# Optimization experiments

Hardware: AMD Instinct MI355X
Metric: run time of the kernel (lower is better)

The kernel has to match this reference:

```python
import jax, jax.numpy as jnp
import numpy as np

B, L, DIM, H, HD = 1, 2048, 2048, 16, 128  # head_dim = DIM // H; RoPE pairs = HD // 2


def setup_inputs() -> dict:
    key = jax.random.key(0)
    ks = jax.random.split(key, 6)
    x = jax.random.normal(ks[0], (B, L, DIM), dtype=jnp.float32)
    pe = jax.random.normal(ks[1], (1, 1, L, HD // 2, 2, 2), dtype=jnp.float32)
    qkv_w = jax.random.normal(ks[2], (3 * DIM, DIM), dtype=jnp.float32) * 0.02
    q_scale = jnp.ones((HD,), dtype=jnp.float32)
    k_scale = jnp.ones((HD,), dtype=jnp.float32)
    proj_w = jax.random.normal(ks[3], (DIM, DIM), dtype=jnp.float32) * 0.02
    proj_b = jnp.zeros((DIM,), dtype=jnp.float32)
    return {"x": x, "pe": pe, "qkv_w": qkv_w, "q_scale": q_scale,
            "k_scale": k_scale, "proj_w": proj_w, "proj_b": proj_b}


def _rmsnorm(t, scale):
    # per-head-dim RMSNorm, eps=1e-6, computed in fp32 (inputs already fp32)
    rrms = jax.lax.rsqrt(jnp.mean(t * t, axis=-1, keepdims=True) + 1e-6)
    return t * rrms * scale


def _apply_rope(q, k, pe):
    def rot(t):
        t_ = t.reshape(*t.shape[:-1], -1, 1, 2)  # [B,H,L,HD/2,1,2]
        out = pe[..., 0] * t_[..., 0] + pe[..., 1] * t_[..., 1]  # [B,H,L,HD/2,2]
        return out.reshape(t.shape)
    return rot(q), rot(k)


def reference(x, pe, qkv_w, q_scale, k_scale, proj_w, proj_b):
    b, l, _ = x.shape
    qkv = jnp.einsum('bld,ed->ble', x, qkv_w)  # [B, L, 3*DIM]
    qkv = qkv.reshape(b, l, 3, H, HD)
    # 'B L (K H D) -> K B H L D'
    qkv = jnp.transpose(qkv, (2, 0, 3, 1, 4))
    q, k, v = qkv[0], qkv[1], qkv[2]  # each [B, H, L, HD]
    q = _rmsnorm(q, q_scale)
    k = _rmsnorm(k, k_scale)
    q, k = _apply_rope(q, k, pe)
    scale = 1.0 / jnp.sqrt(jnp.asarray(HD, dtype=q.dtype))
    scores = jnp.einsum('bhqd,bhkd->bhqk', q, k) * scale
    attn = jax.nn.softmax(scores, axis=-1)
    out = jnp.einsum('bhqk,bhkd->bhqd', attn, v)  # [B, H, L, HD]
    out = jnp.transpose(out, (0, 2, 1, 3)).reshape(b, l, H * HD)  # 'B H L D -> B L (H D)'
    return jnp.einsum('bld,ed->ble', out, proj_w) + proj_b
```

## Files before the change

kernel.cpp:

```cpp
#include <hip/hip_runtime.h>
#include <hip/hip_bf16.h>
#include <math.h>

#define L_SEQ 2048
#define DIM   2048
#define NH    16
#define HD    128
#define TDIM  6144

typedef __attribute__((ext_vector_type(8))) short short8;
typedef __attribute__((ext_vector_type(4))) float f32x4;
typedef __attribute__((ext_vector_type(4))) unsigned int u32x4;

__device__ __forceinline__ void gl_lds16(const void* g, void* l) {
  __builtin_amdgcn_global_load_lds(
      (const __attribute__((address_space(1))) unsigned int*)g,
      (__attribute__((address_space(3))) unsigned int*)l, 16, 0, 0);
}

__device__ __forceinline__ short bf16bits(float x) {
  __hip_bfloat16 h = __float2bfloat16(x);
  return *(short*)&h;
}

__device__ __forceinline__ float bits2f(short s) {
  unsigned int u = ((unsigned int)(unsigned short)s) << 16;
  return __uint_as_float(u);
}

__device__ __forceinline__ unsigned int pack_bf16(float a, float b) {
  __hip_bfloat162 h = __float22bfloat162_rn(make_float2(a, b));
  return *(unsigned int*)&h;
}

__global__ __launch_bounds__(256)
void cast2_bf16(const float* __restrict__ a, __hip_bfloat16* __restrict__ oa,
                const float* __restrict__ b, __hip_bfloat16* __restrict__ ob) {
  int i = (blockIdx.x * 256 + threadIdx.x) * 8;
  const float* src;
  __hip_bfloat16* dst;
  int off;
  if (i < DIM * DIM) { src = a; dst = oa; off = i; }
  else               { src = b; dst = ob; off = i - DIM * DIM; }
  float4 v0 = *(const float4*)(src + off);
  float4 v1 = *(const float4*)(src + off + 4);
  short8 o;
  o[0] = bf16bits(v0.x); o[1] = bf16bits(v0.y); o[2] = bf16bits(v0.z); o[3] = bf16bits(v0.w);
  o[4] = bf16bits(v1.x); o[5] = bf16bits(v1.y); o[6] = bf16bits(v1.z); o[7] = bf16bits(v1.w);
  *(short8*)(dst + off) = o;
}

__global__ __launch_bounds__(256)
void cast_bf16(const float* __restrict__ in, __hip_bfloat16* __restrict__ out, int n) {
  int i = (blockIdx.x * 256 + threadIdx.x) * 8;
  if (i >= n) return;
  float4 a = *(const float4*)(in + i);
  float4 b = *(const float4*)(in + i + 4);
  short8 o;
  o[0] = bf16bits(a.x); o[1] = bf16bits(a.y); o[2] = bf16bits(a.z); o[3] = bf16bits(a.w);
  o[4] = bf16bits(b.x); o[5] = bf16bits(b.y); o[6] = bf16bits(b.z); o[7] = bf16bits(b.w);
  *(short8*)(out + i) = o;
}

#define QKV_N 6144
#define QKV_K 2048

__global__ __launch_bounds__(512, 2)
void gemm_qkv_256(const __hip_bfloat16* __restrict__ A,
                  const __hip_bfloat16* __restrict__ B,
                  __hip_bfloat16* __restrict__ C) {
  extern __shared__ char smem[];
  const int tid  = threadIdx.x;
  const int lane = tid & 63, w = tid >> 6;
  const int l15  = lane & 15, quad = lane >> 4;
  const int wm   = w >> 2, wn = w & 3;

  const int orig = blockIdx.x;
  const int by = orig & 7;
  const int bx = orig >> 3;
  const int m0 = by * 256, n0 = bx * 256;

  const int ar0 = tid >> 2,         aq0 = tid & 3;
  const int ar1 = (512 + tid) >> 2, aq1 = (512 + tid) & 3;
  const __hip_bfloat16* pA0 = A + (size_t)(m0 + ar0) * QKV_K + aq0 * 8;
  const __hip_bfloat16* pA1 = A + (size_t)(m0 + ar1) * QKV_K + aq1 * 8;
  const __hip_bfloat16* pB0 = B + (size_t)(n0 + ar0) * QKV_K + aq0 * 8;
  const __hip_bfloat16* pB1 = B + (size_t)(n0 + ar1) * QKV_K + aq1 * 8;
  const int dst0 = w * 1024;

  f32x4 acc[8][4];
#pragma unroll
  for (int mi = 0; mi < 8; ++mi)
#pragma unroll
    for (int ni = 0; ni < 4; ++ni) acc[mi][ni] = (f32x4){0.f, 0.f, 0.f, 0.f};

  const int aoff = ((wm * 128 + l15) * 32 + quad * 8) * 2;
  const int boff = ((wn * 64 + l15) * 32 + quad * 8) * 2;

#pragma unroll
  for (int p = 0; p < 3; ++p) {
    char* Sp = smem + p * 32768;
    gl_lds16(pA0 + p * 32, Sp + dst0);
    gl_lds16(pA1 + p * 32, Sp + dst0 + 8192);
    gl_lds16(pB0 + p * 32, Sp + 16384 + dst0);
    gl_lds16(pB1 + p * 32, Sp + 16384 + dst0 + 8192);
  }
  asm volatile("s_waitcnt vmcnt(8)\n\ts_barrier" ::: "memory");

  for (int tb = 0; tb < 64; tb += 4) {
#pragma unroll
    for (int u = 0; u < 4; ++u) {
      const int t  = tb + u;
      const char* As = smem + u * 32768;
      const char* Bs = As + 16384;
      const int tn = (t + 3) & 63;
      char* Sn = smem + ((u + 3) & 3) * 32768;

      short8 a[8];
#pragma unroll
      for (int mi = 0; mi < 8; ++mi)
        a[mi] = *(const short8*)(As + aoff + mi * 1024);
      short8 b0 = *(const short8*)(Bs + boff);
      short8 b1 = *(const short8*)(Bs + boff + 1024);
      gl_lds16(pA0 + tn * 32, Sn + dst0);
      gl_lds16(pA1 + tn * 32, Sn + dst0 + 8192);
      __builtin_amdgcn_s_barrier();
      __builtin_amdgcn_s_setprio(1);
#pragma unroll
      for (int mi = 0; mi < 8; ++mi) {
        acc[mi][0] = __builtin_amdgcn_mfma_f32_16x16x32_bf16(a[mi], b0, acc[mi][0], 0, 0, 0);
        acc[mi][1] = __builtin_amdgcn_mfma_f32_16x16x32_bf16(a[mi], b1, acc[mi][1], 0, 0, 0);
      }
      __builtin_amdgcn_s_setprio(0);
      __builtin_amdgcn_s_barrier();

      short8 b2 = *(const short8*)(Bs + boff + 2048);
      short8 b3 = *(const short8*)(Bs + boff + 3072);
      gl_lds16(pB0 + tn * 32, Sn + 16384 + dst0);
      gl_lds16(pB1 + tn * 32, Sn + 16384 + dst0 + 8192);
      asm volatile("s_waitcnt vmcnt(8)\n\ts_barrier" ::: "memory");
      __builtin_amdgcn_s_setprio(1);
#pragma unroll
      for (int mi = 0; mi < 8; ++mi) {
        acc[mi][2] = __builtin_amdgcn_mfma_f32_16x16x32_bf16(a[mi], b2, acc[mi][2], 0, 0, 0);
        acc[mi][3] = __builtin_amdgcn_mfma_f32_16x16x32_bf16(a[mi], b3, acc[mi][3], 0, 0, 0);
      }
      __builtin_amdgcn_s_setprio(0);
      __builtin_amdgcn_s_barrier();
    }
  }

  const int crow = m0 + wm * 128 + quad * 4;
  const int ccol = n0 + wn * 64 + l15;
#pragma unroll
  for (int mi = 0; mi < 8; ++mi)
#pragma unroll
    for (int ni = 0; ni < 4; ++ni)
#pragma unroll
      for (int r = 0; r < 4; ++r)
        C[(size_t)(crow + mi * 16 + r) * QKV_N + ccol + ni * 16] =
            __float2bfloat16(acc[mi][ni][r]);
}

__global__ __launch_bounds__(256)
void qkv_epilogue(const __hip_bfloat16* __restrict__ C,
                  const float* __restrict__ q_scale, const float* __restrict__ k_scale,
                  const float* __restrict__ pe,
                  __hip_bfloat16* __restrict__ Qb, __hip_bfloat16* __restrict__ Kb,
                  __hip_bfloat16* __restrict__ Vt) {
  const int bid = blockIdx.x;
  const int t = threadIdx.x;
  if (bid < 512) {
    const int sec = bid >> 8;
    const int h   = (bid >> 4) & 15;
    const int rb  = bid & 15;
    const float* scale = sec ? k_scale : q_scale;
    const float qmul = sec ? 1.0f : 0.08838834764831845f;
    __hip_bfloat16* dst = sec ? Kb : Qb;

    const int row = t >> 1, half = t & 1;
    const int l = rb * 128 + row;
    const __hip_bfloat16* grow = C + (size_t)l * TDIM + sec * DIM + h * HD + half * 64;

    float ss = 0.f;
#pragma unroll
    for (int c8 = 0; c8 < 64; c8 += 8) {
      short8 v8 = *(const short8*)(grow + c8);
#pragma unroll
      for (int j = 0; j < 8; ++j) { float f = bits2f(v8[j]); ss += f * f; }
    }
    ss += __shfl_xor(ss, 1);
    const float rrms = rsqrtf(ss * (1.f / 128.f) + 1e-6f);

    const float* perow = pe + (size_t)l * 256 + half * 128;
    __hip_bfloat16* drow = dst + ((size_t)h * L_SEQ + l) * HD + half * 64;

#pragma unroll
    for (int c8 = 0; c8 < 64; c8 += 8) {
      short8 v8 = *(const short8*)(grow + c8);
      float f[8];
#pragma unroll
      for (int j = 0; j < 8; ++j)
        f[j] = bits2f(v8[j]) * rrms * scale[half * 64 + c8 + j];
      short8 o;
#pragma unroll
      for (int p = 0; p < 4; ++p) {
        float4 pp = *(const float4*)(perow + c8 * 2 + p * 4);
        float e = f[2 * p], od = f[2 * p + 1];
        o[2 * p]     = bf16bits((pp.x * e + pp.y * od) * qmul);
        o[2 * p + 1] = bf16bits((pp.z * e + pp.w * od) * qmul);
      }
      *(short8*)(drow + c8) = o;
    }
  } else {
    __shared__ short Tt[128 * 72];
    const int vb = bid - 512;
    const int h = vb >> 5, lb = vb & 31;
    const int l0 = lb * 64;
#pragma unroll
    for (int k = 0; k < 4; ++k) {
      int idx = t + k * 256;
      int row = idx >> 4, c = idx & 15;
      short8 v = *(const short8*)(C + (size_t)(l0 + row) * TDIM + 2 * DIM + h * HD + c * 8);
#pragma unroll
      for (int j = 0; j < 8; ++j) Tt[(c * 8 + j) * 72 + row] = v[j];
    }
    __syncthreads();
    const int d = t >> 1, lh = t & 1;
    __hip_bfloat16* vrow = Vt + ((size_t)h * HD + d) * L_SEQ + l0 + lh * 32;
#pragma unroll
    for (int k = 0; k < 4; ++k) {
      short8 o = *(const short8*)&Tt[d * 72 + lh * 32 + k * 8];
      *(short8*)(vrow + k * 8) = o;
    }
  }
}

__global__ __launch_bounds__(256)
void gemm_proj(const __hip_bfloat16* __restrict__ A, const __hip_bfloat16* __restrict__ B,
               const float* __restrict__ bias, float* __restrict__ C,
               int M, int N, int K) {
  const int n0 = blockIdx.x * 128, m0 = blockIdx.y * 128;
  const int t = threadIdx.x, lane = t & 63, w = t >> 6;
  const int l15 = lane & 15, quad = lane >> 4;
  const int wm = (w & 1) * 64, wn = (w >> 1) * 64;

  __shared__ __align__(16) __hip_bfloat16 As[128 * 32];
  __shared__ __align__(16) __hip_bfloat16 Bs[128 * 32];

  f32x4 acc[4][4];
#pragma unroll
  for (int mt = 0; mt < 4; ++mt)
#pragma unroll
    for (int nt = 0; nt < 4; ++nt) acc[mt][nt] = (f32x4){0.f, 0.f, 0.f, 0.f};

  const int arow  = lane >> 2;
  const int acol8 = (lane & 3) * 8;
  const __hip_bfloat16* Ab = A + (size_t)(m0 + w * 16 + arow) * K + acol8;
  const __hip_bfloat16* Bb = B + (size_t)(n0 + w * 16 + arow) * K + acol8;
  __hip_bfloat16* As_base = As + (size_t)(w * 16) * 32;
  __hip_bfloat16* Bs_base = Bs + (size_t)(w * 16) * 32;

  for (int kb = 0; kb < K; kb += 32) {
    gl_lds16(Ab + kb,                As_base);
    gl_lds16(Ab + kb + (size_t)64*K, As_base + 64 * 32);
    gl_lds16(Bb + kb,                Bs_base);
    gl_lds16(Bb + kb + (size_t)64*K, Bs_base + 64 * 32);
    __syncthreads();

    short8 am[4], bn[4];
#pragma unroll
    for (int mt = 0; mt < 4; ++mt)
      am[mt] = *(const short8*)&As[(size_t)(wm + mt*16 + l15) * 32 + quad * 8];
#pragma unroll
    for (int nt = 0; nt < 4; ++nt)
      bn[nt] = *(const short8*)&Bs[(size_t)(wn + nt*16 + l15) * 32 + quad * 8];
#pragma unroll
    for (int mt = 0; mt < 4; ++mt)
#pragma unroll
      for (int nt = 0; nt < 4; ++nt)
        acc[mt][nt] = __builtin_amdgcn_mfma_f32_16x16x32_bf16(am[mt], bn[nt], acc[mt][nt], 0, 0, 0);
    __syncthreads();
  }

#pragma unroll
  for (int mt = 0; mt < 4; ++mt)
#pragma unroll
    for (int nt = 0; nt < 4; ++nt) {
      int col = n0 + wn + nt * 16 + l15;
#pragma unroll
      for (int r = 0; r < 4; ++r) {
        int row = m0 + wm + mt * 16 + quad * 4 + r;
        C[(size_t)row * N + col] = acc[mt][nt][r] + bias[col];
      }
    }
}

#define NZ 4
#define ZLEN (L_SEQ / NZ)

__global__ __launch_bounds__(256, 4)
void attn_mfma(const __hip_bfloat16* __restrict__ Qb,
               const __hip_bfloat16* __restrict__ Kb,
               const __hip_bfloat16* __restrict__ Vt,
               __hip_bfloat16* __restrict__ Opart, float2* __restrict__ ml) {
  const int orig = blockIdx.x;
  const int wg   = (orig & 7) * 256 + (orig >> 3);
  const int h    = wg >> 7;
  const int rem  = wg & 127;
  const int z    = rem >> 5;
  const int q0   = (rem & 31) * 64;
  const int t  = threadIdx.x;
  const int lane = t & 63, w = t >> 6;
  const int l15 = lane & 15, quad = lane >> 4;
  const int sw = l15 & 7;

  __shared__ __align__(16) __hip_bfloat16 Ks[64 * 128];
  __shared__ __align__(16) __hip_bfloat16 Vs[128 * 64];

  const __hip_bfloat16* kbase = Kb + (size_t)h * L_SEQ * HD;
  const __hip_bfloat16* vbase = Vt + (size_t)h * HD * L_SEQ;

  short8 aq[4];
  {
    const __hip_bfloat16* qbase = Qb + ((size_t)h * L_SEQ + q0 + w * 16 + l15) * HD;
#pragma unroll
    for (int ks = 0; ks < 4; ++ks)
      aq[ks] = *(const short8*)(qbase + ks * 32 + quad * 8);
  }

  f32x4 o[8];
#pragma unroll
  for (int n2 = 0; n2 < 8; ++n2) o[n2] = (f32x4){0.f, 0.f, 0.f, 0.f};
  float m_run = -1e30f, l_run = 0.f;

  for (int kt = 0; kt < ZLEN / 64; ++kt) {
    const int k0 = z * ZLEN + kt * 64;
#pragma unroll
    for (int i = 0; i < 4; ++i) {
      int krow = w * 16 + i * 4 + (lane >> 4);
      int kch  = (lane & 15) ^ (krow & 7);
      gl_lds16(kbase + (size_t)(k0 + krow) * HD + kch * 8,
               &Ks[(w * 16 + i * 4) * 128]);
    }
#pragma unroll
    for (int i = 0; i < 4; ++i) {
      int vrow = w * 32 + i * 8 + (lane >> 3);
      int vch  = (lane & 7) ^ (vrow & 7);
      gl_lds16(vbase + (size_t)vrow * L_SEQ + k0 + vch * 8,
               &Vs[(w * 32 + i * 8) * 64]);
    }
    __syncthreads();

    f32x4 s[4];
#pragma unroll
    for (int nt = 0; nt < 4; ++nt) s[nt] = (f32x4){0.f, 0.f, 0.f, 0.f};
    __builtin_amdgcn_s_setprio(1);
#pragma unroll
    for (int ks = 0; ks < 4; ++ks) {
      short8 bk[4];
#pragma unroll
      for (int nt = 0; nt < 4; ++nt)
        bk[nt] = *(const short8*)&Ks[(nt * 16 + l15) * 128 + ((ks * 4 + quad) ^ sw) * 8];
#pragma unroll
      for (int nt = 0; nt < 4; ++nt)
        s[nt] = __builtin_amdgcn_mfma_f32_16x16x32_bf16(bk[nt], aq[ks], s[nt], 0, 0, 0);
    }
    __builtin_amdgcn_s_setprio(0);

    float mx0 = fmaxf(fmaxf(s[0][0], s[0][1]), fmaxf(s[0][2], s[0][3]));
    float mx1 = fmaxf(fmaxf(s[1][0], s[1][1]), fmaxf(s[1][2], s[1][3]));
    float mx2 = fmaxf(fmaxf(s[2][0], s[2][1]), fmaxf(s[2][2], s[2][3]));
    float mx3 = fmaxf(fmaxf(s[3][0], s[3][1]), fmaxf(s[3][2], s[3][3]));
    float rm = fmaxf(fmaxf(mx0, mx1), fmaxf(mx2, mx3));
    rm = fmaxf(rm, __shfl_xor(rm, 16));
    rm = fmaxf(rm, __shfl_xor(rm, 32));

    if (!__all(rm <= m_run + 8.f)) {
      float mnew = fmaxf(m_run, rm);
      float alpha = __expf(m_run - mnew);
      m_run = mnew;
      l_run *= alpha;
      float alpha_r[4];
#pragma unroll
      for (int r = 0; r < 4; ++r) alpha_r[r] = __shfl(alpha, quad * 4 + r);
#pragma unroll
      for (int n2 = 0; n2 < 8; ++n2)
#pragma unroll
        for (int r = 0; r < 4; ++r) o[n2][r] *= alpha_r[r];
    }

    float sum = 0.f;
#pragma unroll
    for (int nt = 0; nt < 4; ++nt)
#pragma unroll
      for (int r = 0; r < 4; ++r) {
        float p = __expf(s[nt][r] - m_run);
        s[nt][r] = p;
        sum += p;
      }
    sum += __shfl_xor(sum, 16);
    sum += __shfl_xor(sum, 32);
    l_run += sum;

    unsigned int pk[4][2];
#pragma unroll
    for (int nt = 0; nt < 4; ++nt) {
      pk[nt][0] = pack_bf16(s[nt][0], s[nt][1]);
      pk[nt][1] = pack_bf16(s[nt][2], s[nt][3]);
    }
    short8 ap[2];
#pragma unroll
    for (int ks2 = 0; ks2 < 2; ++ks2) {
      u32x4 a32;
#pragma unroll
      for (int jp = 0; jp < 4; ++jp) {
        int quad_src = (quad & 1) * 2 + (jp >> 1);
        int src = (quad_src << 4) | l15;
        int rp = jp & 1;
        unsigned int v0 = __shfl((int)pk[2 * ks2 + 0][rp], src);
        unsigned int v1 = __shfl((int)pk[2 * ks2 + 1][rp], src);
        a32[jp] = (quad >> 1) ? v1 : v0;
      }
      ap[ks2] = *(short8*)&a32;
    }

    __builtin_amdgcn_s_setprio(1);
#pragma unroll
    for (int ks2 = 0; ks2 < 2; ++ks2)
#pragma unroll
      for (int n2 = 0; n2 < 8; ++n2) {
        short8 bv = *(const short8*)&Vs[(n2 * 16 + l15) * 64 + ((ks2 * 4 + quad) ^ sw) * 8];
        o[n2] = __builtin_amdgcn_mfma_f32_16x16x32_bf16(ap[ks2], bv, o[n2], 0, 0, 0);
      }
    __builtin_amdgcn_s_setprio(0);

    __syncthreads();
  }

  const size_t rb = (size_t)(z * NH + h) * L_SEQ + q0 + w * 16;
  float linv[4];
#pragma unroll
  for (int r = 0; r < 4; ++r) linv[r] = 1.f / __shfl(l_run, quad * 4 + r);
#pragma unroll
  for (int r = 0; r < 4; ++r) {
    size_t row = rb + quad * 4 + r;
#pragma unroll
    for (int n2 = 0; n2 < 8; ++n2)
      Opart[row * HD + n2 * 16 + l15] = __float2bfloat16(o[n2][r] * linv[r]);
  }
  if (quad == 0) ml[rb + l15] = make_float2(m_run, l_run);
}

__global__ __launch_bounds__(256)
void attn_combine4(const __hip_bfloat16* __restrict__ Opart,
                   const float2* __restrict__ ml,
                   __hip_bfloat16* __restrict__ out) {
  const int h  = blockIdx.y;
  const int q  = blockIdx.x * 16 + (threadIdx.x >> 4);
  const int d8 = (threadIdx.x & 15) * 8;
  size_t idx[NZ];
  float2 a[NZ];
#pragma unroll
  for (int zz = 0; zz < NZ; ++zz) {
    idx[zz] = ((size_t)zz * NH + h) * L_SEQ + q;
    a[zz] = ml[idx[zz]];
  }
  float M = fmaxf(fmaxf(a[0].x, a[1].x), fmaxf(a[2].x, a[3].x));
  float wz[NZ];
  float tot = 0.f;
#pragma unroll
  for (int zz = 0; zz < NZ; ++zz) {
    wz[zz] = __expf(a[zz].x - M) * a[zz].y;
    tot += wz[zz];
  }
  float inv = 1.f / tot;
  float acc[8] = {0.f, 0.f, 0.f, 0.f, 0.f, 0.f, 0.f, 0.f};
#pragma unroll
  for (int zz = 0; zz < NZ; ++zz) {
    short8 ov = *(const short8*)&Opart[idx[zz] * HD + d8];
#pragma unroll
    for (int j = 0; j < 8; ++j) acc[j] += wz[zz] * bits2f(ov[j]);
  }
  short8 r;
#pragma unroll
  for (int j = 0; j < 8; ++j) r[j] = bf16bits(acc[j] * inv);
  *(short8*)&out[(size_t)q * DIM + h * HD + d8] = r;
}

extern "C" void kernel_launch(void* const* d_in, const int* in_sizes, int n_in,
                              void* d_out, int out_size, void* d_ws, size_t ws_size,
                              hipStream_t stream) {
  const float* x       = (const float*)d_in[0];
  const float* pe      = (const float*)d_in[1];
  const float* qkv_w   = (const float*)d_in[2];
  const float* q_scale = (const float*)d_in[3];
  const float* k_scale = (const float*)d_in[4];
  const float* proj_w  = (const float*)d_in[5];
  const float* proj_b  = (const float*)d_in[6];
  float* out = (float*)d_out;

  char* base = (char*)d_ws;
  __hip_bfloat16* xb       = (__hip_bfloat16*)base;
  __hip_bfloat16* wb       = (__hip_bfloat16*)(base + 8388608);
  __hip_bfloat16* Cq       = (__hip_bfloat16*)(base + 33554432);
  __hip_bfloat16* Qb       = (__hip_bfloat16*)base;
  __hip_bfloat16* Kb       = (__hip_bfloat16*)(base + 8388608);
  __hip_bfloat16* Vt       = (__hip_bfloat16*)(base + 16777216);
  __hip_bfloat16* Opart    = (__hip_bfloat16*)(base + 33554432);
  float2*         ml       = (float2*)(base + 25165824);
  __hip_bfloat16* attn_out = (__hip_bfloat16*)base;
  __hip_bfloat16* pwb      = (__hip_bfloat16*)(base + 33554432);

  static bool attr_done = false;
  if (!attr_done) {
    hipFuncSetAttribute((const void*)gemm_qkv_256,
                        hipFuncAttributeMaxDynamicSharedMemorySize, 131072);
    attr_done = true;
  }

  cast2_bf16<<<dim3((DIM * DIM + TDIM * DIM) / (256 * 8)), 256, 0, stream>>>(
      x, xb, qkv_w, wb);

  gemm_qkv_256<<<dim3((TDIM / 256) * (L_SEQ / 256)), 512, 131072, stream>>>(xb, wb, Cq);

  qkv_epilogue<<<dim3(1024), 256, 0, stream>>>(Cq, q_scale, k_scale, pe, Qb, Kb, Vt);

  attn_mfma<<<dim3(NZ * NH * (L_SEQ / 64)), 256, 0, stream>>>(Qb, Kb, Vt, Opart, ml);

  attn_combine4<<<dim3(L_SEQ / 16, NH), 256, 0, stream>>>(Opart, ml, attn_out);

  cast_bf16<<<dim3(DIM * DIM / (256 * 8)), 256, 0, stream>>>(proj_w, pwb, DIM * DIM);

  gemm_proj<<<dim3(DIM / 128, DIM / 128), 256, 0, stream>>>(
      attn_out, pwb, proj_b, out, L_SEQ, DIM, DIM);
}
```

Measured before the change: 329.1 us.

## Switch attention to 32x32x16 MFMA with 128-row query tiles and permlane swap

The attention kernel now uses 32x32x16 bf16 MFMAs instead of 16x16x32, and each wave owns 32 query rows, so a block covers 128 queries and the grid is halved. The P-to-A-operand conversion uses v_permlane32_swap instead of several shuffles, and one lane owns one query row, which removes most cross-lane reductions. The output is staged through LDS so each row goes to global memory as coalesced 16-byte stores. Each block now reuses every K/V tile for twice as many queries, but register pressure rises and occupancy is lowered to 3 blocks per CU.

Result: faster. 318.6 us (-3.2%).

```diff
diff --git a/kernel.cpp b/kernel.cpp
--- a/kernel.cpp
+++ b/kernel.cpp
@@ -10,6 +10,7 @@
 
 typedef __attribute__((ext_vector_type(8))) short short8;
 typedef __attribute__((ext_vector_type(4))) float f32x4;
+typedef __attribute__((ext_vector_type(16))) float f32x16;
 typedef __attribute__((ext_vector_type(4))) unsigned int u32x4;
 
 __device__ __forceinline__ void gl_lds16(const void* g, void* l) {
@@ -299,21 +300,21 @@
 #define NZ 4
 #define ZLEN (L_SEQ / NZ)
 
-__global__ __launch_bounds__(256, 4)
+__global__ __launch_bounds__(256, 3)
 void attn_mfma(const __hip_bfloat16* __restrict__ Qb,
                const __hip_bfloat16* __restrict__ Kb,
                const __hip_bfloat16* __restrict__ Vt,
                __hip_bfloat16* __restrict__ Opart, float2* __restrict__ ml) {
   const int orig = blockIdx.x;
-  const int wg   = (orig & 7) * 256 + (orig >> 3);
-  const int h    = wg >> 7;
-  const int rem  = wg & 127;
-  const int z    = rem >> 5;
-  const int q0   = (rem & 31) * 64;
-  const int t  = threadIdx.x;
+  const int wg   = (orig & 7) * 128 + (orig >> 3);
+  const int h    = wg >> 6;
+  const int rem  = wg & 63;
+  const int z    = rem >> 4;
+  const int q0   = (rem & 15) * 128;
+  const int t    = threadIdx.x;
   const int lane = t & 63, w = t >> 6;
-  const int l15 = lane & 15, quad = lane >> 4;
-  const int sw = l15 & 7;
+  const int l31  = lane & 31;
+  const int u    = lane >> 5;
 
   __shared__ __align__(16) __hip_bfloat16 Ks[64 * 128];
   __shared__ __align__(16) __hip_bfloat16 Vs[128 * 64];
@@ -321,17 +322,19 @@
   const __hip_bfloat16* kbase = Kb + (size_t)h * L_SEQ * HD;
   const __hip_bfloat16* vbase = Vt + (size_t)h * HD * L_SEQ;
 
-  short8 aq[4];
+  short8 aq[8];
   {
-    const __hip_bfloat16* qbase = Qb + ((size_t)h * L_SEQ + q0 + w * 16 + l15) * HD;
-#pragma unroll
-    for (int ks = 0; ks < 4; ++ks)
-      aq[ks] = *(const short8*)(qbase + ks * 32 + quad * 8);
-  }
-
-  f32x4 o[8];
-#pragma unroll
-  for (int n2 = 0; n2 < 8; ++n2) o[n2] = (f32x4){0.f, 0.f, 0.f, 0.f};
+    const __hip_bfloat16* qb = Qb + ((size_t)h * L_SEQ + q0 + w * 32 + l31) * HD + u * 8;
+#pragma unroll
+    for (int hh = 0; hh < 8; ++hh)
+      aq[hh] = *(const short8*)(qb + hh * 16);
+  }
+
+  f32x16 o[4];
+#pragma unroll
+  for (int dt = 0; dt < 4; ++dt)
+#pragma unroll
+    for (int r = 0; r < 16; ++r) o[dt][r] = 0.f;
   float m_run = -1e30f, l_run = 0.f;
 
   for (int kt = 0; kt < ZLEN / 64; ++kt) {
@@ -352,104 +355,105 @@
     }
     __syncthreads();
 
-    f32x4 s[4];
-#pragma unroll
-    for (int nt = 0; nt < 4; ++nt) s[nt] = (f32x4){0.f, 0.f, 0.f, 0.f};
-    __builtin_amdgcn_s_setprio(1);
-#pragma unroll
-    for (int ks = 0; ks < 4; ++ks) {
-      short8 bk[4];
-#pragma unroll
-      for (int nt = 0; nt < 4; ++nt)
-        bk[nt] = *(const short8*)&Ks[(nt * 16 + l15) * 128 + ((ks * 4 + quad) ^ sw) * 8];
-#pragma unroll
-      for (int nt = 0; nt < 4; ++nt)
-        s[nt] = __builtin_amdgcn_mfma_f32_16x16x32_bf16(bk[nt], aq[ks], s[nt], 0, 0, 0);
-    }
-    __builtin_amdgcn_s_setprio(0);
-
-    float mx0 = fmaxf(fmaxf(s[0][0], s[0][1]), fmaxf(s[0][2], s[0][3]));
-    float mx1 = fmaxf(fmaxf(s[1][0], s[1][1]), fmaxf(s[1][2], s[1][3]));
-    float mx2 = fmaxf(fmaxf(s[2][0], s[2][1]), fmaxf(s[2][2], s[2][3]));
-    float mx3 = fmaxf(fmaxf(s[3][0], s[3][1]), fmaxf(s[3][2], s[3][3]));
-    float rm = fmaxf(fmaxf(mx0, mx1), fmaxf(mx2, mx3));
-    rm = fmaxf(rm, __shfl_xor(rm, 16));
-    rm = fmaxf(rm, __shfl_xor(rm, 32));
-
-    if (!__all(rm <= m_run + 8.f)) {
-      float mnew = fmaxf(m_run, rm);
-      float alpha = __expf(m_run - mnew);
-      m_run = mnew;
-      l_run *= alpha;
-      float alpha_r[4];
-#pragma unroll
-      for (int r = 0; r < 4; ++r) alpha_r[r] = __shfl(alpha, quad * 4 + r);
-#pragma unroll
-      for (int n2 = 0; n2 < 8; ++n2)
-#pragma unroll
-        for (int r = 0; r < 4; ++r) o[n2][r] *= alpha_r[r];
-    }
-
-    float sum = 0.f;
-#pragma unroll
-    for (int nt = 0; nt < 4; ++nt)
-#pragma unroll
-      for (int r = 0; r < 4; ++r) {
-        float p = __expf(s[nt][r] - m_run);
-        s[nt][r] = p;
+#pragma unroll
+    for (int ks = 0; ks < 2; ++ks) {
+      const int krow = ks * 32 + l31;
+      const char* krowp = (const char*)Ks + krow * 256;
+      const int ksw = krow & 7;
+      f32x16 s;
+#pragma unroll
+      for (int r = 0; r < 16; ++r) s[r] = 0.f;
+      __builtin_amdgcn_s_setprio(1);
+#pragma unroll
+      for (int hh = 0; hh < 8; ++hh) {
+        short8 ak = *(const short8*)(krowp + ((hh * 2 + u) ^ ksw) * 16);
+        s = __builtin_amdgcn_mfma_f32_32x32x16_bf16(ak, aq[hh], s, 0, 0, 0);
+      }
+      __builtin_amdgcn_s_setprio(0);
+
+      float rm = s[0];
+#pragma unroll
+      for (int r = 1; r < 16; ++r) rm = fmaxf(rm, s[r]);
+      rm = fmaxf(rm, __shfl_xor(rm, 32));
+
+      if (!__all(rm <= m_run + 8.f)) {
+        float mnew = fmaxf(m_run, rm);
+        float alpha = __expf(m_run - mnew);
+        m_run = mnew;
+        l_run *= alpha;
+#pragma unroll
+        for (int dt = 0; dt < 4; ++dt)
+#pragma unroll
+          for (int r = 0; r < 16; ++r) o[dt][r] *= alpha;
+      }
+
+      float sum = 0.f;
+#pragma unroll
+      for (int r = 0; r < 16; ++r) {
+        float p = __expf(s[r] - m_run);
+        s[r] = p;
         sum += p;
       }
-    sum += __shfl_xor(sum, 16);
-    sum += __shfl_xor(sum, 32);
-    l_run += sum;
-
-    unsigned int pk[4][2];
-#pragma unroll
-    for (int nt = 0; nt < 4; ++nt) {
-      pk[nt][0] = pack_bf16(s[nt][0], s[nt][1]);
-      pk[nt][1] = pack_bf16(s[nt][2], s[nt][3]);
-    }
-    short8 ap[2];
-#pragma unroll
-    for (int ks2 = 0; ks2 < 2; ++ks2) {
-      u32x4 a32;
-#pragma unroll
-      for (int jp = 0; jp < 4; ++jp) {
-        int quad_src = (quad & 1) * 2 + (jp >> 1);
-        int src = (quad_src << 4) | l15;
-        int rp = jp & 1;
-        unsigned int v0 = __shfl((int)pk[2 * ks2 + 0][rp], src);
-        unsigned int v1 = __shfl((int)pk[2 * ks2 + 1][rp], src);
-        a32[jp] = (quad >> 1) ? v1 : v0;
-      }
-      ap[ks2] = *(short8*)&a32;
-    }
-
-    __builtin_amdgcn_s_setprio(1);
-#pragma unroll
-    for (int ks2 = 0; ks2 < 2; ++ks2)
-#pragma unroll
-      for (int n2 = 0; n2 < 8; ++n2) {
-        short8 bv = *(const short8*)&Vs[(n2 * 16 + l15) * 64 + ((ks2 * 4 + quad) ^ sw) * 8];
-        o[n2] = __builtin_amdgcn_mfma_f32_16x16x32_bf16(ap[ks2], bv, o[n2], 0, 0, 0);
-      }
-    __builtin_amdgcn_s_setprio(0);
-
+      sum += __shfl_xor(sum, 32);
+      l_run += sum;
+
+      unsigned int W0 = pack_bf16(s[0],  s[1]),  W1 = pack_bf16(s[2],  s[3]);
+      unsigned int W2 = pack_bf16(s[4],  s[5]),  W3 = pack_bf16(s[6],  s[7]);
+      unsigned int W4 = pack_bf16(s[8],  s[9]),  W5 = pack_bf16(s[10], s[11]);
+      unsigned int W6 = pack_bf16(s[12], s[13]), W7 = pack_bf16(s[14], s[15]);
+      asm("v_permlane32_swap_b32 %0, %1" : "+v"(W0), "+v"(W2));
+      asm("v_permlane32_swap_b32 %0, %1" : "+v"(W1), "+v"(W3));
+      asm("v_permlane32_swap_b32 %0, %1" : "+v"(W4), "+v"(W6));
+      asm("v_permlane32_swap_b32 %0, %1" : "+v"(W5), "+v"(W7));
+      u32x4 pb0 = {W0, W1, W2, W3};
+      u32x4 pb1 = {W4, W5, W6, W7};
+      short8 ap0 = *(short8*)&pb0;
+      short8 ap1 = *(short8*)&pb1;
+
+      __builtin_amdgcn_s_setprio(1);
+#pragma unroll
+      for (int dt = 0; dt < 4; ++dt) {
+        const int d = dt * 32 + l31;
+        const char* vrowp = (const char*)Vs + d * 128;
+        const int vsw = d & 7;
+        short8 av0 = *(const short8*)(vrowp + ((ks * 4 + u) ^ vsw) * 16);
+        o[dt] = __builtin_amdgcn_mfma_f32_32x32x16_bf16(av0, ap0, o[dt], 0, 0, 0);
+        short8 av1 = *(const short8*)(vrowp + ((ks * 4 + 2 + u) ^ vsw) * 16);
+        o[dt] = __builtin_amdgcn_mfma_f32_32x32x16_bf16(av1, ap1, o[dt], 0, 0, 0);
+      }
+      __builtin_amdgcn_s_setprio(0);
+    }
     __syncthreads();
   }
 
-  const size_t rb = (size_t)(z * NH + h) * L_SEQ + q0 + w * 16;
-  float linv[4];
-#pragma unroll
-  for (int r = 0; r < 4; ++r) linv[r] = 1.f / __shfl(l_run, quad * 4 + r);
-#pragma unroll
-  for (int r = 0; r < 4; ++r) {
-    size_t row = rb + quad * 4 + r;
-#pragma unroll
-    for (int n2 = 0; n2 < 8; ++n2)
-      Opart[row * HD + n2 * 16 + l15] = __float2bfloat16(o[n2][r] * linv[r]);
-  }
-  if (quad == 0) ml[rb + l15] = make_float2(m_run, l_run);
+  const float linv = 1.f / l_run;
+  char* Ot = (char*)Ks + w * 8192;
+  const int qsw = l31 & 7;
+#pragma unroll
+  for (int dt = 0; dt < 4; ++dt)
+#pragma unroll
+    for (int p = 0; p < 8; ++p) {
+      unsigned int v = pack_bf16(o[dt][2 * p] * linv, o[dt][2 * p + 1] * linv);
+      int dpair = dt * 16 + (p & 1) + (p >> 1) * 4 + 2 * u;
+      *(unsigned int*)(Ot + l31 * 256 + ((dpair >> 2) ^ qsw) * 16 + (dpair & 3) * 4) = v;
+    }
+  __syncthreads();
+  {
+    const int qr = lane >> 1, half = lane & 1;
+    const char* Orow = (char*)Ks + w * 8192 + qr * 256;
+    __hip_bfloat16* gout =
+        Opart + ((size_t)(z * NH + h) * L_SEQ + q0 + w * 32 + qr) * HD;
+#pragma unroll
+    for (int c8 = 0; c8 < 8; ++c8) {
+      int chunk = half * 8 + c8;
+      short8 v = *(const short8*)(Orow + ((chunk ^ (qr & 7)) * 16));
+      *(short8*)(gout + chunk * 8) = v;
+    }
+  }
+  if (lane < 32) {
+    size_t rb = (size_t)(z * NH + h) * L_SEQ + q0 + w * 32;
+    ml[rb + l31] = make_float2(m_run, l_run);
+  }
 }
 
 __global__ __launch_bounds__(256)
@@ -526,7 +530,7 @@
 
   qkv_epilogue<<<dim3(1024), 256, 0, stream>>>(Cq, q_scale, k_scale, pe, Qb, Kb, Vt);
 
-  attn_mfma<<<dim3(NZ * NH * (L_SEQ / 64)), 256, 0, stream>>>(Qb, Kb, Vt, Opart, ml);
+  attn_mfma<<<dim3(NZ * NH * (L_SEQ / 128)), 256, 0, stream>>>(Qb, Kb, Vt, Opart, ml);
 
   attn_combine4<<<dim3(L_SEQ / 16, NH), 256, 0, stream>>>(Opart, ml, attn_out);
 
```
